# Kernel tuning notes

Measured on AMD Instinct MI355X. Metric: run time of the kernel, lower is better.

Reference implementation:

```python
import jax, jax.numpy as jnp
import numpy as np
from jax import lax

B, P, N, D, L, H = 16, 8192, 1024, 384, 12, 6
HD = D // H
K_NEI = 5          # HomogeneityLoss k
KL_RATIO = 1.0


def setup_inputs() -> dict:
    key = jax.random.key(0)
    ks = jax.random.split(key, 10)
    s = lambda i, shape, sc=0.02: (jax.random.normal(ks[i], shape, jnp.float32) * sc)
    return dict(
        pts=jax.random.normal(ks[0], (B, P, 3), jnp.float32),
        grid=jax.random.normal(ks[1], (B, N, 3), jnp.float32),
        embed_w=s(2, (3, D), 0.1),
        proj_w=s(3, (D, 3), 0.1),
        ln1_w=jnp.ones((L, D)), ln1_b=jnp.zeros((L, D)),
        qkv_w=s(4, (L, D, 3 * D)), qkv_b=jnp.zeros((L, 3 * D)),
        attn_w=s(5, (L, D, D)), attn_b=jnp.zeros((L, D)),
        ln2_w=jnp.ones((L, D)), ln2_b=jnp.zeros((L, D)),
        mlp_w1=s(6, (L, D, 4 * D)), mlp_b1=jnp.zeros((L, 4 * D)),
        mlp_w2=s(7, (L, 4 * D, D)), mlp_b2=jnp.zeros((L, D)),
    )


def _ln(x, w, b):
    m = jnp.mean(x, -1, keepdims=True)
    v = jnp.var(x, -1, keepdims=True)
    return (x - m) * lax.rsqrt(v + 1e-5) * w + b


def _transformer(x, params):
    def layer(x, p):
        l1w, l1b, qw, qb, aw, ab, l2w, l2b, m1w, m1b, m2w, m2b = p
        h = _ln(x, l1w, l1b)
        qkv = h @ qw + qb                                   # [B,N,3D]
        q, k, v = jnp.split(qkv, 3, axis=-1)
        rs = lambda t: t.reshape(B, N, H, HD).transpose(0, 2, 1, 3)  # [B,H,N,HD]
        q, k, v = rs(q), rs(k), rs(v)
        att = jax.nn.softmax(jnp.einsum('bhnd,bhmd->bhnm', q, k) / np.sqrt(HD), axis=-1)
        o = jnp.einsum('bhnm,bhmd->bhnd', att, v).transpose(0, 2, 1, 3).reshape(B, N, D)
        x = x + (o @ aw + ab)
        h = _ln(x, l2w, l2b)
        x = x + (jax.nn.gelu(h @ m1w + m1b) @ m2w + m2b)
        return x, None
    x, _ = lax.scan(layer, x, params)
    return x


def _fps(points):  # points: [P,3] -> N int32 indices (farthest point sampling)
    def body(carry, _):
        dists, last = carry
        d = jnp.sum((points - points[last]) ** 2, axis=-1)
        dists = jnp.minimum(dists, d)
        return (dists, jnp.argmax(dists).astype(jnp.int32)), last
    init = (jnp.full((points.shape[0],), 1e10, points.dtype), jnp.int32(0))
    (_, _), idxs = lax.scan(body, init, None, length=N)
    return idxs


def reference(pts, grid, embed_w, proj_w, ln1_w, ln1_b, qkv_w, qkv_b,
              attn_w, attn_b, ln2_w, ln2_b, mlp_w1, mlp_b1, mlp_w2, mlp_b2):
    params = (ln1_w, ln1_b, qkv_w, qkv_b, attn_w, attn_b,
              ln2_w, ln2_b, mlp_w1, mlp_b1, mlp_w2, mlp_b2)
    x = grid @ embed_w                                      # [B,N,D]
    x = _transformer(x, params)
    pred = x @ proj_w                                       # [B,N,3]

    # FPS centers from the raw point cloud
    idxs = jax.vmap(_fps)(pts)                              # [B,N]
    centers = jnp.take_along_axis(pts, idxs[..., None], axis=1)  # [B,N,3]

    # Chamfer L1 (symmetric mean of nearest-neighbor L2 norms)
    d = jnp.linalg.norm(pred[:, :, None, :] - centers[:, None, :, :], axis=-1)  # [B,N,N]
    rec = 0.5 * (d.min(axis=2).mean(axis=1) + d.min(axis=1).mean(axis=1))       # [B]

    # Homogeneity: mean dist of K_NEI nearest neighbors -> softmax -> KL(q||p)
    dd = jnp.linalg.norm(pred[:, :, None, :] - pred[:, None, :, :], axis=-1)    # [B,N,N]
    neg_vals, _ = lax.top_k(-dd, K_NEI + 1)                 # smallest K+1 dists
    mean_d = (-neg_vals[..., 1:]).mean(axis=-1)             # drop self -> [B,N]
    logp = jax.nn.log_softmax(mean_d, axis=-1)
    q = 1.0 / N
    kl = jnp.sum(q * (jnp.log(q) - logp), axis=-1)          # [B]

    return rec.mean(), KL_RATIO * kl.mean()
```

## Files before the change

### kernel.cpp

```cpp
#include <hip/hip_runtime.h>
#include <math.h>

#define B_   16
#define P_   8192
#define N_   1024
#define D_   384
#define L_   12
#define H_   6
#define HD_  64
#define M_   (B_*N_)
#define DQKV_ (3*D_)
#define DH_   (4*D_)

typedef unsigned short ushort_t;
typedef unsigned long long u64_t;
typedef __attribute__((ext_vector_type(8))) short short8;
typedef __attribute__((ext_vector_type(4))) float floatx4;

__device__ __forceinline__ ushort_t f2bf(float f) {
    unsigned u = __float_as_uint(f);
    unsigned rounding = 0x7fffu + ((u >> 16) & 1u);
    return (ushort_t)((u + rounding) >> 16);
}
__device__ __forceinline__ float bf2f(ushort_t u) {
    return __uint_as_float(((unsigned)u) << 16);
}

__global__ __launch_bounds__(D_) void embed_kernel(const float* __restrict__ g,
                                                   const float* __restrict__ ew,
                                                   float* __restrict__ X) {
    int m = blockIdx.x;
    int d = threadIdx.x;
    float g0 = g[m*3+0], g1 = g[m*3+1], g2 = g[m*3+2];
    X[(size_t)m*D_ + d] = g0*ew[0*D_+d] + g1*ew[1*D_+d] + g2*ew[2*D_+d];
}

__global__ __launch_bounds__(256) void transcast_kernel(const float* __restrict__ W,
                                                        ushort_t* __restrict__ Wt,
                                                        int K, int Nc) {
    __shared__ float t[32][33];
    const float* Wl = W + (size_t)blockIdx.z*K*Nc;
    ushort_t* Wtl = Wt + (size_t)blockIdx.z*K*Nc;
    int n0 = blockIdx.x*32, k0 = blockIdx.y*32;
    int tx = threadIdx.x & 31, ty = threadIdx.x >> 5;
#pragma unroll
    for (int j = 0; j < 32; j += 8)
        t[ty+j][tx] = Wl[(size_t)(k0+ty+j)*Nc + n0+tx];
    __syncthreads();
#pragma unroll
    for (int j = 0; j < 32; j += 8)
        Wtl[(size_t)(n0+ty+j)*K + k0+tx] = f2bf(t[tx][ty+j]);
}

__global__ __launch_bounds__(256) void ln_kernel(const float* __restrict__ Xin,
                                                 const float* __restrict__ w,
                                                 const float* __restrict__ bvec,
                                                 ushort_t* __restrict__ out) {
    int wid = threadIdx.x >> 6, lane = threadIdx.x & 63;
    int row = blockIdx.x*4 + wid;
    const float* xr = Xin + (size_t)row*D_;
    float v[6];
#pragma unroll
    for (int i = 0; i < 6; i++) v[i] = xr[lane + i*64];
    float s = 0.f;
#pragma unroll
    for (int i = 0; i < 6; i++) s += v[i];
#pragma unroll
    for (int off = 32; off; off >>= 1) s += __shfl_xor(s, off, 64);
    float mean = s * (1.0f/(float)D_);
    float vs = 0.f;
#pragma unroll
    for (int i = 0; i < 6; i++) { float d = v[i]-mean; vs += d*d; }
#pragma unroll
    for (int off = 32; off; off >>= 1) vs += __shfl_xor(vs, off, 64);
    float var = vs * (1.0f/(float)D_);
    float rstd = 1.0f / sqrtf(var + 1e-5f);
    ushort_t* orow = out + (size_t)row*D_;
#pragma unroll
    for (int i = 0; i < 6; i++) {
        int e = lane + i*64;
        orow[e] = f2bf((v[i]-mean)*rstd*w[e] + bvec[e]);
    }
}

__device__ __forceinline__ float gelu_f(float x) {
    const float c = 0.7978845608028654f;
    float x3 = x*x*x;
    return 0.5f*x*(1.0f + tanhf(c*(x + 0.044715f*x3)));
}

template<int EPI>
__global__ __launch_bounds__(256) void mfma_gemm(const ushort_t* __restrict__ A,
                                                 const ushort_t* __restrict__ Wt,
                                                 const float* __restrict__ bias,
                                                 void* __restrict__ Cout,
                                                 ushort_t* __restrict__ VT,
                                                 int K, int Nc) {
    __shared__ __attribute__((aligned(16))) ushort_t smem[2*128*32];
    ushort_t* smA = smem;
    ushort_t* smB = smem + 128*32;
    int tid = threadIdx.x;
    int lane = tid & 63, w = tid >> 6;
    int wm = w >> 1, wn = w & 1;
    int L = lane & 15, G = lane >> 4;
    int rowBase = blockIdx.y * 128, colBase = blockIdx.x * 128;

    floatx4 acc[4][4];
#pragma unroll
    for (int i = 0; i < 4; i++)
#pragma unroll
        for (int j = 0; j < 4; j++) acc[i][j] = (floatx4){0.f,0.f,0.f,0.f};

    int sr = tid >> 2;
    int kc = tid & 3;
    const ushort_t* Ag = A  + (size_t)(rowBase + sr)*K + kc*8;
    const ushort_t* Bg = Wt + (size_t)(colBase + sr)*K + kc*8;
    size_t step64 = (size_t)64*K;

    short8 ra0, ra1, rb0, rb1;
    ra0 = *(const short8*)(Ag);
    ra1 = *(const short8*)(Ag + step64);
    rb0 = *(const short8*)(Bg);
    rb1 = *(const short8*)(Bg + step64);

    for (int k0 = 0; k0 < K; k0 += 32) {
        __syncthreads();
        *(short8*)(smA + sr*32 + kc*8)        = ra0;
        *(short8*)(smA + (64+sr)*32 + kc*8)   = ra1;
        *(short8*)(smB + sr*32 + kc*8)        = rb0;
        *(short8*)(smB + (64+sr)*32 + kc*8)   = rb1;
        __syncthreads();
        if (k0 + 32 < K) {
            ra0 = *(const short8*)(Ag + k0 + 32);
            ra1 = *(const short8*)(Ag + step64 + k0 + 32);
            rb0 = *(const short8*)(Bg + k0 + 32);
            rb1 = *(const short8*)(Bg + step64 + k0 + 32);
        }
        short8 af[4], bfr[4];
#pragma unroll
        for (int t = 0; t < 4; t++) {
            af[t]  = *(const short8*)(smA + (wm*64 + t*16 + L)*32 + G*8);
            bfr[t] = *(const short8*)(smB + (wn*64 + t*16 + L)*32 + G*8);
        }
#pragma unroll
        for (int mt = 0; mt < 4; mt++)
#pragma unroll
            for (int nt = 0; nt < 4; nt++)
                acc[mt][nt] = __builtin_amdgcn_mfma_f32_16x16x32_bf16(
                    af[mt], bfr[nt], acc[mt][nt], 0, 0, 0);
        __syncthreads();
    }

    __syncthreads();

    if (EPI == 3 && colBase >= 2*D_) {
        int cBase = colBase + wn*64 + L;
        int rBase = rowBase + wm*64 + G*4;
#pragma unroll
        for (int nt = 0; nt < 4; nt++) {
            int col = cBase + nt*16;
            float bv = bias[col];
            int hh = (col - 2*D_) >> 6, d = (col - 2*D_) & 63;
#pragma unroll
            for (int mt = 0; mt < 4; mt++) {
#pragma unroll
                for (int r = 0; r < 4; r++) {
                    int row = rBase + mt*16 + r;
                    int b = row >> 10, n = row & 1023;
                    VT[(((size_t)b*H_ + hh)*64 + d)*N_ + n] = f2bf(acc[mt][nt][r] + bv);
                }
            }
        }
    } else if (EPI == 1) {
        float* fs = (float*)smem + w*1024;
        int orow = lane >> 2, c4 = lane & 3;
#pragma unroll
        for (int mt = 0; mt < 4; mt++) {
#pragma unroll
            for (int nt = 0; nt < 4; nt++) {
                float bv = bias[colBase + wn*64 + nt*16 + L];
#pragma unroll
                for (int r = 0; r < 4; r++)
                    fs[(G*4+r)*64 + nt*16 + L] = acc[mt][nt][r] + bv;
            }
            float* og = (float*)Cout + (size_t)(rowBase + wm*64 + mt*16 + orow)*Nc
                        + colBase + wn*64;
#pragma unroll
            for (int kk = 0; kk < 4; kk++) {
                float4 sv = *(float4*)(fs + orow*64 + kk*16 + c4*4);
                float4 gv = *(float4*)(og + kk*16 + c4*4);
                gv.x += sv.x; gv.y += sv.y; gv.z += sv.z; gv.w += sv.w;
                *(float4*)(og + kk*16 + c4*4) = gv;
            }
        }
    } else {
        ushort_t* us = smem + w*1152;
        int orow = lane >> 2, oc = lane & 3;
#pragma unroll
        for (int mt = 0; mt < 4; mt++) {
#pragma unroll
            for (int nt = 0; nt < 4; nt++) {
                float bv = bias[colBase + wn*64 + nt*16 + L];
#pragma unroll
                for (int r = 0; r < 4; r++) {
                    float v = acc[mt][nt][r] + bv;
                    if (EPI == 2) v = gelu_f(v);
                    us[(G*4+r)*72 + nt*16 + L] = f2bf(v);
                }
            }
            short8 o0 = *(short8*)(us + orow*72 + oc*8);
            short8 o1 = *(short8*)(us + orow*72 + 32 + oc*8);
            ushort_t* og = (ushort_t*)Cout + (size_t)(rowBase + wm*64 + mt*16 + orow)*Nc
                           + colBase + wn*64;
            *(short8*)(og + oc*8) = o0;
            *(short8*)(og + 32 + oc*8) = o1;
        }
    }
}

#define LPAD 72
__global__ __launch_bounds__(256) void fattn_kernel(const ushort_t* __restrict__ QKV,
                                                    const ushort_t* __restrict__ VT,
                                                    ushort_t* __restrict__ O) {
    __shared__ __attribute__((aligned(16))) ushort_t Ks[64*LPAD];
    __shared__ __attribute__((aligned(16))) ushort_t Vs[64*LPAD];
    __shared__ __attribute__((aligned(16))) ushort_t Pw[4*16*LPAD];
    int b = blockIdx.z, h = blockIdx.y;
    int qBase = blockIdx.x * 64;
    int tid = threadIdx.x;
    int lane = tid & 63, w = tid >> 6;
    int L = lane & 15, G = lane >> 4;

    short8 qf[2];
    {
        const ushort_t* qp = QKV + ((size_t)(b*N_ + qBase + w*16 + L))*DQKV_ + h*HD_ + G*8;
        qf[0] = *(const short8*)(qp);
        qf[1] = *(const short8*)(qp + 32);
    }

    floatx4 oacc[4];
#pragma unroll
    for (int nt = 0; nt < 4; nt++) oacc[nt] = (floatx4){0.f,0.f,0.f,0.f};
    float mrow[4], lrow[4];
#pragma unroll
    for (int r = 0; r < 4; r++) { mrow[r] = -3.0e38f; lrow[r] = 0.f; }

    ushort_t* pw = Pw + w*16*LPAD;
    const ushort_t* Kbase = QKV + (size_t)b*N_*DQKV_ + D_ + h*HD_;
    const ushort_t* Vbase = VT + ((size_t)b*H_ + h)*64*N_;

    int srow = tid >> 3;
    int dc   = tid & 7;
    const ushort_t* Kg0 = Kbase + (size_t)srow*DQKV_ + dc*8;
    const ushort_t* Kg1 = Kbase + (size_t)(srow+32)*DQKV_ + dc*8;
    const ushort_t* Vg0 = Vbase + (size_t)srow*N_ + dc*8;
    const ushort_t* Vg1 = Vbase + (size_t)(srow+32)*N_ + dc*8;

    short8 rk0, rk1, rv0, rv1;
    rk0 = *(const short8*)(Kg0);
    rk1 = *(const short8*)(Kg1);
    rv0 = *(const short8*)(Vg0);
    rv1 = *(const short8*)(Vg1);

    for (int kt = 0; kt < N_/64; kt++) {
        __syncthreads();
        *(short8*)(Ks + srow*LPAD + dc*8)       = rk0;
        *(short8*)(Ks + (srow+32)*LPAD + dc*8)  = rk1;
        *(short8*)(Vs + srow*LPAD + dc*8)       = rv0;
        *(short8*)(Vs + (srow+32)*LPAD + dc*8)  = rv1;
        __syncthreads();
        if (kt + 1 < N_/64) {
            rk0 = *(const short8*)(Kg0 + (size_t)(kt+1)*64*DQKV_);
            rk1 = *(const short8*)(Kg1 + (size_t)(kt+1)*64*DQKV_);
            rv0 = *(const short8*)(Vg0 + (kt+1)*64);
            rv1 = *(const short8*)(Vg1 + (kt+1)*64);
        }

        floatx4 sc[4];
#pragma unroll
        for (int ct = 0; ct < 4; ct++) sc[ct] = (floatx4){0.f,0.f,0.f,0.f};
#pragma unroll
        for (int ks = 0; ks < 2; ks++)
#pragma unroll
            for (int ct = 0; ct < 4; ct++) {
                short8 bf = *(const short8*)(Ks + (ct*16 + L)*LPAD + ks*32 + G*8);
                sc[ct] = __builtin_amdgcn_mfma_f32_16x16x32_bf16(qf[ks], bf, sc[ct], 0, 0, 0);
            }

        float rmax[4], rsum[4];
#pragma unroll
        for (int r = 0; r < 4; r++) {
#pragma unroll
            for (int ct = 0; ct < 4; ct++) sc[ct][r] *= 0.125f;
            rmax[r] = fmaxf(fmaxf(sc[0][r], sc[1][r]), fmaxf(sc[2][r], sc[3][r]));
        }
#pragma unroll
        for (int off = 1; off < 16; off <<= 1)
#pragma unroll
            for (int r = 0; r < 4; r++) rmax[r] = fmaxf(rmax[r], __shfl_xor(rmax[r], off, 64));
        float corr[4];
#pragma unroll
        for (int r = 0; r < 4; r++) {
            float mn = fmaxf(mrow[r], rmax[r]);
            corr[r] = __expf(mrow[r] - mn);
            mrow[r] = mn;
            rsum[r] = 0.f;
#pragma unroll
            for (int ct = 0; ct < 4; ct++) {
                float p = __expf(sc[ct][r] - mn);
                sc[ct][r] = p;
                rsum[r] += p;
            }
        }
#pragma unroll
        for (int off = 1; off < 16; off <<= 1)
#pragma unroll
            for (int r = 0; r < 4; r++) rsum[r] += __shfl_xor(rsum[r], off, 64);
#pragma unroll
        for (int r = 0; r < 4; r++) lrow[r] = lrow[r]*corr[r] + rsum[r];

#pragma unroll
        for (int ct = 0; ct < 4; ct++)
#pragma unroll
            for (int r = 0; r < 4; r++)
                pw[(G*4 + r)*LPAD + ct*16 + L] = f2bf(sc[ct][r]);
#pragma unroll
        for (int nt = 0; nt < 4; nt++)
#pragma unroll
            for (int r = 0; r < 4; r++) oacc[nt][r] *= corr[r];

#pragma unroll
        for (int ks = 0; ks < 2; ks++) {
            short8 pf = *(const short8*)(pw + L*LPAD + ks*32 + G*8);
#pragma unroll
            for (int nt = 0; nt < 4; nt++) {
                short8 vf = *(const short8*)(Vs + (nt*16 + L)*LPAD + ks*32 + G*8);
                oacc[nt] = __builtin_amdgcn_mfma_f32_16x16x32_bf16(pf, vf, oacc[nt], 0, 0, 0);
            }
        }
    }

    float inv[4];
#pragma unroll
    for (int r = 0; r < 4; r++) inv[r] = 1.0f / lrow[r];
#pragma unroll
    for (int nt = 0; nt < 4; nt++)
#pragma unroll
        for (int r = 0; r < 4; r++)
            pw[(G*4 + r)*LPAD + nt*16 + L] = f2bf(oacc[nt][r]*inv[r]);
    int orow = lane >> 2, oc = lane & 3;
    short8 o0 = *(short8*)(pw + orow*LPAD + oc*8);
    short8 o1 = *(short8*)(pw + orow*LPAD + 32 + oc*8);
    ushort_t* og = O + (size_t)(b*N_ + qBase + w*16 + orow)*D_ + h*HD_;
    *(short8*)(og + oc*8) = o0;
    *(short8*)(og + 32 + oc*8) = o1;
}

__global__ __launch_bounds__(256) void proj_kernel(const float* __restrict__ X,
                                                   const float* __restrict__ pw,
                                                   float* __restrict__ pred) {
    int wid = threadIdx.x >> 6, lane = threadIdx.x & 63;
    int m = blockIdx.x*4 + wid;
    const float* xr = X + (size_t)m*D_;
    float a0 = 0.f, a1 = 0.f, a2 = 0.f;
#pragma unroll
    for (int i = 0; i < 6; i++) {
        int k = lane + i*64;
        float xv = xr[k];
        a0 += xv*pw[k*3+0]; a1 += xv*pw[k*3+1]; a2 += xv*pw[k*3+2];
    }
#pragma unroll
    for (int off = 32; off; off >>= 1) {
        a0 += __shfl_xor(a0, off, 64);
        a1 += __shfl_xor(a1, off, 64);
        a2 += __shfl_xor(a2, off, 64);
    }
    if (lane == 0) {
        pred[m*3+0] = a0; pred[m*3+1] = a1; pred[m*3+2] = a2;
    }
}

template<int CTRL>
__device__ __forceinline__ u64_t dpp_max64(u64_t x) {
    unsigned lo = (unsigned)x;
    unsigned hi = (unsigned)(x >> 32);
    lo = (unsigned)__builtin_amdgcn_update_dpp((int)lo, (int)lo, CTRL, 0xF, 0xF, false);
    hi = (unsigned)__builtin_amdgcn_update_dpp((int)hi, (int)hi, CTRL, 0xF, 0xF, false);
    u64_t o = ((u64_t)hi << 32) | lo;
    return (o > x) ? o : x;
}
__device__ __forceinline__ u64_t swz16_max64(u64_t x) {
    unsigned lo = (unsigned)x;
    unsigned hi = (unsigned)(x >> 32);
    lo = (unsigned)__builtin_amdgcn_ds_swizzle((int)lo, 0x401F);
    hi = (unsigned)__builtin_amdgcn_ds_swizzle((int)hi, 0x401F);
    u64_t o = ((u64_t)hi << 32) | lo;
    return (o > x) ? o : x;
}

__global__ __launch_bounds__(512) void fps_kernel(const float* __restrict__ pts,
                                                  float* __restrict__ centers) {
    __shared__ float Lx[P_], Ly[P_], Lz[P_];
    __shared__ u64_t slot[2][32];
    int b = blockIdx.x, t = threadIdx.x;
    const float* pb = pts + (size_t)b*P_*3;
    float px[16], py[16], pz[16], dist[16];
#pragma unroll
    for (int j = 0; j < 16; j++) {
        int p = j*512 + t;
        px[j] = pb[p*3+0]; py[j] = pb[p*3+1]; pz[j] = pb[p*3+2];
        Lx[p] = px[j]; Ly[p] = py[j]; Lz[p] = pz[j];
        dist[j] = 1e10f;
    }
    int winner = 0;
    __syncthreads();
    for (int it = 0; it < N_; it++) {
        float lx = Lx[winner], ly = Ly[winner], lz = Lz[winner];
        if (t == 0) {
            float* c = centers + ((size_t)b*N_ + it)*3;
            c[0] = lx; c[1] = ly; c[2] = lz;
        }
        float bd = -1.0f; int bj = 0;
#pragma unroll
        for (int j = 0; j < 16; j++) {
            float dx = __fsub_rn(px[j], lx);
            float dy = __fsub_rn(py[j], ly);
            float dz = __fsub_rn(pz[j], lz);
            float d = __fadd_rn(__fadd_rn(__fmul_rn(dx,dx), __fmul_rn(dy,dy)), __fmul_rn(dz,dz));
            d = fminf(dist[j], d);
            dist[j] = d;
            bool gt = d > bd;
            bd = gt ? d : bd;
            bj = gt ? j : bj;
        }
        u64_t best = ((u64_t)__float_as_uint(bd) << 32)
                   | (unsigned)(~(unsigned)(bj*512 + t));
        best = dpp_max64<0xB1>(best);
        best = dpp_max64<0x4E>(best);
        best = dpp_max64<0x124>(best);
        best = dpp_max64<0x128>(best);
        int par = it & 1;
        if ((t & 15) == 0) slot[par][t >> 4] = best;
        __syncthreads();
        u64_t v = slot[par][t & 31];
        v = dpp_max64<0xB1>(v);
        v = dpp_max64<0x4E>(v);
        v = dpp_max64<0x124>(v);
        v = dpp_max64<0x128>(v);
        v = swz16_max64(v);
        winner = (int)(~(unsigned)(v & 0xFFFFFFFFull));
    }
}

__global__ __launch_bounds__(256) void nnmin_kernel(const float* __restrict__ Asrc,
                                                    const float* __restrict__ Bsrc,
                                                    float* __restrict__ outmin) {
    int b = blockIdx.y;
    int i = blockIdx.x*256 + threadIdx.x;
    __shared__ float tile[256][3];
    const float* ar = Asrc + ((size_t)b*N_ + i)*3;
    float ax = ar[0], ay = ar[1], az = ar[2];
    float best = 3.0e38f;
    for (int j0 = 0; j0 < N_; j0 += 256) {
        __syncthreads();
        const float* br = Bsrc + ((size_t)b*N_ + j0 + threadIdx.x)*3;
        tile[threadIdx.x][0] = br[0]; tile[threadIdx.x][1] = br[1]; tile[threadIdx.x][2] = br[2];
        __syncthreads();
        for (int j = 0; j < 256; j++) {
            float dx = ax - tile[j][0], dy = ay - tile[j][1], dz = az - tile[j][2];
            float d = dx*dx + dy*dy + dz*dz;
            best = fminf(best, d);
        }
    }
    outmin[(size_t)b*N_ + i] = sqrtf(best);
}

__global__ __launch_bounds__(256) void knn_kernel(const float* __restrict__ Pp,
                                                  float* __restrict__ mean_d) {
    int b = blockIdx.y;
    int i = blockIdx.x*256 + threadIdx.x;
    __shared__ float tile[256][3];
    const float* ar = Pp + ((size_t)b*N_ + i)*3;
    float ax = ar[0], ay = ar[1], az = ar[2];
    float s[6];
#pragma unroll
    for (int q = 0; q < 6; q++) s[q] = 3.0e38f;
    for (int j0 = 0; j0 < N_; j0 += 256) {
        __syncthreads();
        const float* br = Pp + ((size_t)b*N_ + j0 + threadIdx.x)*3;
        tile[threadIdx.x][0] = br[0]; tile[threadIdx.x][1] = br[1]; tile[threadIdx.x][2] = br[2];
        __syncthreads();
        for (int j = 0; j < 256; j++) {
            float dx = ax - tile[j][0], dy = ay - tile[j][1], dz = az - tile[j][2];
            float d = dx*dx + dy*dy + dz*dz;
            if (d < s[5]) {
                s[5] = d;
#pragma unroll
                for (int q = 5; q > 0; q--)
                    if (s[q] < s[q-1]) { float tmp = s[q]; s[q] = s[q-1]; s[q-1] = tmp; }
            }
        }
    }
    float msum = sqrtf(s[1]) + sqrtf(s[2]) + sqrtf(s[3]) + sqrtf(s[4]) + sqrtf(s[5]);
    mean_d[(size_t)b*N_ + i] = msum * 0.2f;
}

__global__ __launch_bounds__(256) void kl_kernel(const float* __restrict__ md,
                                                 float* __restrict__ klb) {
    int b = blockIdx.x, t = threadIdx.x;
    const float* row = md + (size_t)b*N_;
    float v[4];
#pragma unroll
    for (int i = 0; i < 4; i++) v[i] = row[t + i*256];
    float mx = fmaxf(fmaxf(v[0], v[1]), fmaxf(v[2], v[3]));
#pragma unroll
    for (int off = 32; off; off >>= 1) mx = fmaxf(mx, __shfl_xor(mx, off, 64));
    __shared__ float redm[4], rse[4], rsx[4];
    int wid = t >> 6, lane = t & 63;
    if (lane == 0) redm[wid] = mx;
    __syncthreads();
    mx = fmaxf(fmaxf(redm[0], redm[1]), fmaxf(redm[2], redm[3]));
    float se = 0.f, sx = 0.f;
#pragma unroll
    for (int i = 0; i < 4; i++) { se += expf(v[i]-mx); sx += v[i]; }
#pragma unroll
    for (int off = 32; off; off >>= 1) { se += __shfl_xor(se, off, 64); sx += __shfl_xor(sx, off, 64); }
    if (lane == 0) { rse[wid] = se; rsx[wid] = sx; }
    __syncthreads();
    if (t == 0) {
        float SE = rse[0]+rse[1]+rse[2]+rse[3];
        float SX = rsx[0]+rsx[1]+rsx[2]+rsx[3];
        klb[b] = mx + logf(SE) - SX*(1.0f/(float)N_) - logf((float)N_);
    }
}

__global__ __launch_bounds__(256) void final_kernel(const float* __restrict__ rma,
                                                    const float* __restrict__ rmb,
                                                    const float* __restrict__ klb,
                                                    float* __restrict__ out) {
    int t = threadIdx.x;
    float s = 0.f;
    for (int i = t; i < B_*N_; i += 256) s += rma[i] + rmb[i];
#pragma unroll
    for (int off = 32; off; off >>= 1) s += __shfl_xor(s, off, 64);
    __shared__ float red[4];
    int wid = t >> 6, lane = t & 63;
    if (lane == 0) red[wid] = s;
    __syncthreads();
    if (t == 0) {
        float S = red[0]+red[1]+red[2]+red[3];
        out[0] = 0.5f*S/(float)(B_*N_);
        out[1] = 0.f;
        float K = 0.f;
        for (int b = 0; b < B_; b++) K += klb[b];
        out[1] = K/(float)B_;
    }
}

extern "C" void kernel_launch(void* const* d_in, const int* in_sizes, int n_in,
                              void* d_out, int out_size, void* d_ws, size_t ws_size,
                              hipStream_t stream) {
    (void)in_sizes; (void)n_in; (void)out_size; (void)ws_size;
    const float* pts     = (const float*)d_in[0];
    const float* grid    = (const float*)d_in[1];
    const float* embed_w = (const float*)d_in[2];
    const float* proj_w  = (const float*)d_in[3];
    const float* ln1_w   = (const float*)d_in[4];
    const float* ln1_b   = (const float*)d_in[5];
    const float* qkv_w   = (const float*)d_in[6];
    const float* qkv_b   = (const float*)d_in[7];
    const float* attn_w  = (const float*)d_in[8];
    const float* attn_b  = (const float*)d_in[9];
    const float* ln2_w   = (const float*)d_in[10];
    const float* ln2_b   = (const float*)d_in[11];
    const float* mlp_w1  = (const float*)d_in[12];
    const float* mlp_b1  = (const float*)d_in[13];
    const float* mlp_w2  = (const float*)d_in[14];
    const float* mlp_b2  = (const float*)d_in[15];
    float* out = (float*)d_out;

    float*    X     = (float*)d_ws;
    ushort_t* Hb16  = (ushort_t*)(X + (size_t)M_*D_);
    ushort_t* BIG16 = Hb16 + (size_t)M_*D_;
    ushort_t* VT    = BIG16 + (size_t)M_*DH_;
    ushort_t* WQ    = VT  + (size_t)B_*H_*HD_*N_;
    ushort_t* WA    = WQ  + (size_t)L_*DQKV_*D_;
    ushort_t* WM1   = WA  + (size_t)L_*D_*D_;
    ushort_t* WM2   = WM1 + (size_t)L_*DH_*D_;
    float*    PRED  = (float*)(WM2 + (size_t)L_*D_*DH_);
    float*    CENT  = PRED + (size_t)M_*3;
    float*    RMA   = CENT + (size_t)B_*N_*3;
    float*    RMB   = RMA  + (size_t)B_*N_;
    float*    MEAND = RMB  + (size_t)B_*N_;
    float*    KLB   = MEAND + (size_t)B_*N_;

    transcast_kernel<<<dim3(DQKV_/32, D_/32,  L_), 256, 0, stream>>>(qkv_w,  WQ,  D_,  DQKV_);
    transcast_kernel<<<dim3(D_/32,    D_/32,  L_), 256, 0, stream>>>(attn_w, WA,  D_,  D_);
    transcast_kernel<<<dim3(DH_/32,   D_/32,  L_), 256, 0, stream>>>(mlp_w1, WM1, D_,  DH_);
    transcast_kernel<<<dim3(D_/32,    DH_/32, L_), 256, 0, stream>>>(mlp_w2, WM2, DH_, D_);

    fps_kernel<<<B_, 512, 0, stream>>>(pts, CENT);

    embed_kernel<<<M_, D_, 0, stream>>>(grid, embed_w, X);

    for (int l = 0; l < L_; l++) {
        ln_kernel<<<M_/4, 256, 0, stream>>>(X, ln1_w + l*D_, ln1_b + l*D_, Hb16);
        mfma_gemm<3><<<dim3(DQKV_/128, M_/128), 256, 0, stream>>>(
            Hb16, WQ + (size_t)l*DQKV_*D_, qkv_b + l*DQKV_, BIG16, VT, D_, DQKV_);
        fattn_kernel<<<dim3(N_/64, H_, B_), 256, 0, stream>>>(BIG16, VT, Hb16);
        mfma_gemm<1><<<dim3(D_/128, M_/128), 256, 0, stream>>>(
            Hb16, WA + (size_t)l*D_*D_, attn_b + l*D_, X, nullptr, D_, D_);
        ln_kernel<<<M_/4, 256, 0, stream>>>(X, ln2_w + l*D_, ln2_b + l*D_, Hb16);
        mfma_gemm<2><<<dim3(DH_/128, M_/128), 256, 0, stream>>>(
            Hb16, WM1 + (size_t)l*DH_*D_, mlp_b1 + l*DH_, BIG16, nullptr, D_, DH_);
        mfma_gemm<1><<<dim3(D_/128, M_/128), 256, 0, stream>>>(
            BIG16, WM2 + (size_t)l*D_*DH_, mlp_b2 + l*D_, X, nullptr, DH_, D_);
    }

    proj_kernel<<<M_/4, 256, 0, stream>>>(X, proj_w, PRED);

    nnmin_kernel<<<dim3(N_/256, B_), 256, 0, stream>>>(PRED, CENT, RMA);
    nnmin_kernel<<<dim3(N_/256, B_), 256, 0, stream>>>(CENT, PRED, RMB);
    knn_kernel<<<dim3(N_/256, B_), 256, 0, stream>>>(PRED, MEAND);
    kl_kernel<<<B_, 256, 0, stream>>>(MEAND, KLB);
    final_kernel<<<1, 256, 0, stream>>>(RMA, RMB, KLB, out);
}
```

Before: 4.288 ms.

## Widen FPS to 1024 threads with packed-f32 distance math and buffered center writes

```diff
diff --git a/kernel.cpp b/kernel.cpp
--- a/kernel.cpp
+++ b/kernel.cpp
@@ -16,6 +16,7 @@
 typedef unsigned long long u64_t;
 typedef __attribute__((ext_vector_type(8))) short short8;
 typedef __attribute__((ext_vector_type(4))) float floatx4;
+typedef __attribute__((ext_vector_type(2))) float floatx2;
 
 __device__ __forceinline__ ushort_t f2bf(float f) {
     unsigned u = __float_as_uint(f);
@@ -397,19 +398,37 @@
     u64_t o = ((u64_t)hi << 32) | lo;
     return (o > x) ? o : x;
 }
-
-__global__ __launch_bounds__(512) void fps_kernel(const float* __restrict__ pts,
-                                                  float* __restrict__ centers) {
+__device__ __forceinline__ floatx2 pk_sub(floatx2 a, floatx2 b) {
+    floatx2 r;
+    asm("v_pk_add_f32 %0, %1, %2 neg_lo:[0,1] neg_hi:[0,1]" : "=v"(r) : "v"(a), "v"(b));
+    return r;
+}
+__device__ __forceinline__ floatx2 pk_mul(floatx2 a, floatx2 b) {
+    floatx2 r;
+    asm("v_pk_mul_f32 %0, %1, %2" : "=v"(r) : "v"(a), "v"(b));
+    return r;
+}
+__device__ __forceinline__ floatx2 pk_add(floatx2 a, floatx2 b) {
+    floatx2 r;
+    asm("v_pk_add_f32 %0, %1, %2" : "=v"(r) : "v"(a), "v"(b));
+    return r;
+}
+
+__global__ __launch_bounds__(1024) void fps_kernel(const float* __restrict__ pts,
+                                                   float* __restrict__ centers) {
     __shared__ float Lx[P_], Ly[P_], Lz[P_];
-    __shared__ u64_t slot[2][32];
+    __shared__ float Cbuf[N_*3];
+    __shared__ u64_t slot[2][64];
     int b = blockIdx.x, t = threadIdx.x;
     const float* pb = pts + (size_t)b*P_*3;
-    float px[16], py[16], pz[16], dist[16];
-#pragma unroll
-    for (int j = 0; j < 16; j++) {
-        int p = j*512 + t;
-        px[j] = pb[p*3+0]; py[j] = pb[p*3+1]; pz[j] = pb[p*3+2];
-        Lx[p] = px[j]; Ly[p] = py[j]; Lz[p] = pz[j];
+    floatx2 px[4], py[4], pz[4];
+    float dist[8];
+#pragma unroll
+    for (int j = 0; j < 8; j++) {
+        int p = j*1024 + t;
+        float x = pb[p*3+0], y = pb[p*3+1], z = pb[p*3+2];
+        Lx[p] = x; Ly[p] = y; Lz[p] = z;
+        px[j>>1][j&1] = x; py[j>>1][j&1] = y; pz[j>>1][j&1] = z;
         dist[j] = 1e10f;
     }
     int winner = 0;
@@ -417,24 +436,25 @@
     for (int it = 0; it < N_; it++) {
         float lx = Lx[winner], ly = Ly[winner], lz = Lz[winner];
         if (t == 0) {
-            float* c = centers + ((size_t)b*N_ + it)*3;
-            c[0] = lx; c[1] = ly; c[2] = lz;
-        }
+            Cbuf[it*3+0] = lx; Cbuf[it*3+1] = ly; Cbuf[it*3+2] = lz;
+        }
+        floatx2 lx2 = {lx, lx}, ly2 = {ly, ly}, lz2 = {lz, lz};
         float bd = -1.0f; int bj = 0;
 #pragma unroll
-        for (int j = 0; j < 16; j++) {
-            float dx = __fsub_rn(px[j], lx);
-            float dy = __fsub_rn(py[j], ly);
-            float dz = __fsub_rn(pz[j], lz);
-            float d = __fadd_rn(__fadd_rn(__fmul_rn(dx,dx), __fmul_rn(dy,dy)), __fmul_rn(dz,dz));
-            d = fminf(dist[j], d);
-            dist[j] = d;
-            bool gt = d > bd;
-            bd = gt ? d : bd;
-            bj = gt ? j : bj;
+        for (int jj = 0; jj < 4; jj++) {
+            floatx2 dx = pk_sub(px[jj], lx2);
+            floatx2 dy = pk_sub(py[jj], ly2);
+            floatx2 dz = pk_sub(pz[jj], lz2);
+            floatx2 d2 = pk_add(pk_add(pk_mul(dx,dx), pk_mul(dy,dy)), pk_mul(dz,dz));
+            float d0 = fminf(dist[2*jj+0], d2[0]);
+            dist[2*jj+0] = d0;
+            bool g0 = d0 > bd; bd = g0 ? d0 : bd; bj = g0 ? 2*jj+0 : bj;
+            float d1 = fminf(dist[2*jj+1], d2[1]);
+            dist[2*jj+1] = d1;
+            bool g1 = d1 > bd; bd = g1 ? d1 : bd; bj = g1 ? 2*jj+1 : bj;
         }
         u64_t best = ((u64_t)__float_as_uint(bd) << 32)
-                   | (unsigned)(~(unsigned)(bj*512 + t));
+                   | (unsigned)(~(unsigned)((bj<<10) + t));
         best = dpp_max64<0xB1>(best);
         best = dpp_max64<0x4E>(best);
         best = dpp_max64<0x124>(best);
@@ -442,7 +462,9 @@
         int par = it & 1;
         if ((t & 15) == 0) slot[par][t >> 4] = best;
         __syncthreads();
-        u64_t v = slot[par][t & 31];
+        u64_t v0 = slot[par][t & 31];
+        u64_t v1 = slot[par][(t & 31) + 32];
+        u64_t v = (v1 > v0) ? v1 : v0;
         v = dpp_max64<0xB1>(v);
         v = dpp_max64<0x4E>(v);
         v = dpp_max64<0x124>(v);
@@ -450,6 +472,10 @@
         v = swz16_max64(v);
         winner = (int)(~(unsigned)(v & 0xFFFFFFFFull));
     }
+    __syncthreads();
+    float* cb = centers + (size_t)b*N_*3;
+#pragma unroll
+    for (int i = 0; i < 3; i++) cb[t + i*1024] = Cbuf[t + i*1024];
 }
 
 __global__ __launch_bounds__(256) void nnmin_kernel(const float* __restrict__ Asrc,
@@ -599,7 +625,7 @@
     transcast_kernel<<<dim3(DH_/32,   D_/32,  L_), 256, 0, stream>>>(mlp_w1, WM1, D_,  DH_);
     transcast_kernel<<<dim3(D_/32,    DH_/32, L_), 256, 0, stream>>>(mlp_w2, WM2, DH_, D_);
 
-    fps_kernel<<<B_, 512, 0, stream>>>(pts, CENT);
+    fps_kernel<<<B_, 1024, 0, stream>>>(pts, CENT);
 
     embed_kernel<<<M_, D_, 0, stream>>>(grid, embed_w, X);
 
```

After: 4.623 ms. 7.8% more time.
